# Performance work log

Measured on AMD Instinct MI355X. Metric: run time of the kernel, lower is better.

Reference implementation:

```python
import jax, jax.numpy as jnp
import numpy as np
import math

N, E, H, NB, NL, NG, NELEM = 50000, 800000, 64, 8, 2, 64, 100
CUTOFF = 5.0


def _lin(k, fin, fout):
    kw, kb = jax.random.split(k)
    bound = 1.0 / math.sqrt(fin)
    w = jax.random.uniform(kw, (fin, fout), jnp.float32, -bound, bound)
    b = jax.random.uniform(kb, (fout,), jnp.float32, -bound, bound)
    return w, b


def setup_inputs() -> dict:
    key = jax.random.key(0)
    ks = jax.random.split(key, 12)
    z = jax.random.randint(ks[0], (N,), 0, NELEM)
    pos = jax.random.normal(ks[1], (N, 3), jnp.float32)
    edge_index = jax.random.randint(ks[2], (2, E), 0, N)
    batch = jnp.sort(jax.random.randint(ks[3], (N,), 0, NG))
    embed = jax.random.normal(ks[4], (NELEM, H), jnp.float32)
    # stacked per-interaction MLP params, leading dim = NL
    msg_w1, msg_b1, msg_w2, msg_b2 = [], [], [], []
    upd_w1, upd_b1, upd_w2, upd_b2 = [], [], [], []
    for l in range(NL):
        kl = jax.random.fold_in(ks[5], l)
        k1, k2, k3, k4 = jax.random.split(kl, 4)
        w, b = _lin(k1, 2 * H + NB, H); msg_w1.append(w); msg_b1.append(b)
        w, b = _lin(k2, H, H); msg_w2.append(w); msg_b2.append(b)
        w, b = _lin(k3, 2 * H, H); upd_w1.append(w); upd_b1.append(b)
        w, b = _lin(k4, H, H); upd_w2.append(w); upd_b2.append(b)
    eh_w1, eh_b1 = _lin(ks[6], H, H)
    eh_w2, eh_b2 = _lin(ks[7], H, 1)
    return {
        "z": z, "pos": pos, "edge_index": edge_index, "batch": batch,
        "embed": embed,
        "msg_w1": jnp.stack(msg_w1), "msg_b1": jnp.stack(msg_b1),
        "msg_w2": jnp.stack(msg_w2), "msg_b2": jnp.stack(msg_b2),
        "upd_w1": jnp.stack(upd_w1), "upd_b1": jnp.stack(upd_b1),
        "upd_w2": jnp.stack(upd_w2), "upd_b2": jnp.stack(upd_b2),
        "eh_w1": eh_w1, "eh_b1": eh_b1, "eh_w2": eh_w2, "eh_b2": eh_b2,
    }


def _mace_energy(pos, embed, msg_w1, msg_b1, msg_w2, msg_b2,
                 upd_w1, upd_b1, upd_w2, upd_b2,
                 eh_w1, eh_b1, eh_w2, eh_b2,
                 z, edge_index, batch):
    row, col = edge_index[0], edge_index[1]
    edge_vec = pos[row] - pos[col]                      # (E,3)
    d = jnp.linalg.norm(edge_vec, axis=-1)              # (E,)
    env = jnp.where(d < CUTOFF,
                    jnp.cos(d * (math.pi / (2 * CUTOFF))) ** 2,
                    0.0)
    freqs = jnp.arange(1, NB + 1, dtype=pos.dtype) * (math.pi / CUTOFF)
    d_safe = jnp.where(d > 0, d, 1.0)[:, None]
    edge_attr = jnp.sin(freqs * d[:, None]) / d_safe * env[:, None]  # (E,NB)

    x = embed[z]                                        # (N,H)
    for l in range(NL):
        # PyG source_to_target: x_j = x[row], x_i = x[col], aggregate at col
        msg_in = jnp.concatenate([x[col], x[row], edge_attr], axis=-1)  # (E,2H+NB)
        m = jax.nn.silu(msg_in @ msg_w1[l] + msg_b1[l]) @ msg_w2[l] + msg_b2[l]
        agg = jax.ops.segment_sum(m, col, num_segments=N)               # (N,H)
        u_in = jnp.concatenate([x, agg], axis=-1)
        upd = jax.nn.silu(u_in @ upd_w1[l] + upd_b1[l]) @ upd_w2[l] + upd_b2[l]
        x = x + upd

    atomic_e = jax.nn.silu(x @ eh_w1 + eh_b1) @ eh_w2 + eh_b2           # (N,1)
    energy = jax.ops.segment_sum(atomic_e, batch, num_segments=NG)      # (NG,1)
    return energy.squeeze(-1)


def reference(z, pos, edge_index, batch, embed,
              msg_w1, msg_b1, msg_w2, msg_b2,
              upd_w1, upd_b1, upd_w2, upd_b2,
              eh_w1, eh_b1, eh_w2, eh_b2):
    return _mace_energy(pos, embed, msg_w1, msg_b1, msg_w2, msg_b2,
                        upd_w1, upd_b1, upd_w2, upd_b2,
                        eh_w1, eh_b1, eh_w2, eh_b2,
                        z, edge_index, batch)
```

## Files before the change

kernel.cpp:

```cpp
#include <hip/hip_runtime.h>
#include <math.h>

#define NN 50000
#define EE 800000
#define HH 64
#define NBASIS 8
#define NLAYER 2
#define NGRAPH 64
#define NBLK1 49

using half2_t = decltype(__builtin_amdgcn_cvt_pkrtz(0.0f, 0.0f));
typedef _Float16 f16x8 __attribute__((ext_vector_type(8)));
typedef float f32x4 __attribute__((ext_vector_type(4)));

union U4H8 { uint4 u; f16x8 h; };

__device__ __forceinline__ float silu_f(float v) {
    return v * (1.0f / (1.0f + __expf(-v)));
}

__device__ __forceinline__ unsigned pk2(float a, float b) {
    union { half2_t h; unsigned u; } x;
    x.h = __builtin_amdgcn_cvt_pkrtz(a, b);
    return x.u;
}

__device__ __forceinline__ half2_t u2h(unsigned u) {
    union { unsigned u; half2_t h; } x; x.u = u; return x.h;
}

__global__ __launch_bounds__(256) void prep_k(
    const int* __restrict__ z, const float* __restrict__ embed,
    unsigned* __restrict__ xh,
    const float* __restrict__ msg_w1, const float* __restrict__ msg_w2,
    const float* __restrict__ upd_w1, const float* __restrict__ upd_w2,
    const float* __restrict__ eh_w1,
    unsigned* __restrict__ w1t, unsigned* __restrict__ w2t,
    unsigned* __restrict__ w1tu, unsigned* __restrict__ w2tu,
    unsigned* __restrict__ ehw1t,
    const int* __restrict__ ecol, int* __restrict__ deg,
    float4* __restrict__ agg4)
{
    int b = blockIdx.x;
    if (b < 6250) {
        int idx = b * 256 + threadIdx.x;
        int n = idx >> 5;
        int p = idx & 31;
        const float2* er = (const float2*)(embed + ((size_t)z[n] << 6));
        float2 v = er[p];
        xh[idx] = pk2(v.x, v.y);
    } else if (b < 6362) {
        int idx = (b - 6250) * 256 + threadIdx.x;
        if (idx < 10240) {
            int l = idx / 5120, rem = idx % 5120;
            int f = rem / 80, kp = rem % 80;
            const float* w = msg_w1 + (size_t)l * 136 * 64;
            unsigned v = 0;
            if (kp < 68) v = pk2(w[(2*kp)*64 + f], w[(2*kp+1)*64 + f]);
            w1t[idx] = v;
        } else if (idx < 14336) {
            int j = idx - 10240;
            int l = j / 2048, rem = j % 2048;
            int n = rem / 32, kp = rem % 32;
            const float* w = msg_w2 + (size_t)l * 64 * 64;
            w2t[j] = pk2(w[(2*kp)*64 + n], w[(2*kp+1)*64 + n]);
        } else if (idx < 22528) {
            int j = idx - 14336;
            int l = j / 4096, rem = j % 4096;
            int f = rem >> 6, kp = rem & 63;
            const float* w = upd_w1 + (size_t)l * 128 * 64;
            w1tu[j] = pk2(w[(2*kp)*64 + f], w[(2*kp+1)*64 + f]);
        } else if (idx < 26624) {
            int j = idx - 22528;
            int l = j / 2048, rem = j % 2048;
            int n = rem / 32, kp = rem % 32;
            const float* w = upd_w2 + (size_t)l * 64 * 64;
            w2tu[j] = pk2(w[(2*kp)*64 + n], w[(2*kp+1)*64 + n]);
        } else if (idx < 28672) {
            int j = idx - 26624;
            int f = j / 32, kp = j % 32;
            ehw1t[j] = pk2(eh_w1[(2*kp)*64 + f], eh_w1[(2*kp+1)*64 + f]);
        }
    } else if (b < 9487) {
        int e = (b - 6362) * 256 + threadIdx.x;
        if (e < EE) atomicAdd(&deg[ecol[e]], 1);
    } else {
        int idx = (b - 9487) * 256 + threadIdx.x;
        if (idx < NN * 16) {
            float4 z4; z4.x = z4.y = z4.z = z4.w = 0.0f;
            agg4[idx] = z4;
        }
    }
}

__global__ __launch_bounds__(1024) void scan1_k(
    const int* __restrict__ deg, int* __restrict__ cursor,
    int* __restrict__ bsum)
{
    __shared__ int wsum[16];
    int t = threadIdx.x, lane = t & 63, wave = t >> 6;
    int i = blockIdx.x * 1024 + t;
    int v = (i < NN) ? deg[i] : 0;
    int s = v;
#pragma unroll
    for (int off = 1; off < 64; off <<= 1) {
        int tv = __shfl_up(s, off, 64);
        if (lane >= off) s += tv;
    }
    if (lane == 63) wsum[wave] = s;
    __syncthreads();
    if (wave == 0) {
        int ws = (lane < 16) ? wsum[lane] : 0;
        int ss = ws;
#pragma unroll
        for (int off = 1; off < 16; off <<= 1) {
            int tv = __shfl_up(ss, off, 64);
            if (lane >= off) ss += tv;
        }
        if (lane < 16) wsum[lane] = ss - ws;
    }
    __syncthreads();
    int excl = wsum[wave] + s - v;
    if (i < NN) cursor[i] = excl;
    if (t == 1023) bsum[blockIdx.x] = excl + v;
}

__global__ __launch_bounds__(64) void scan2_k(int* __restrict__ bsum)
{
    int lane = threadIdx.x;
    int v = (lane < NBLK1) ? bsum[lane] : 0;
    int s = v;
#pragma unroll
    for (int off = 1; off < 64; off <<= 1) {
        int tv = __shfl_up(s, off, 64);
        if (lane >= off) s += tv;
    }
    if (lane < NBLK1) bsum[lane] = s - v;
}

__global__ __launch_bounds__(256) void scatter_k(
    const int* __restrict__ erow, const int* __restrict__ ecol,
    const float* __restrict__ pos,
    int* __restrict__ cursor, const int* __restrict__ bsum,
    uint2* __restrict__ edgeS)
{
    int e = blockIdx.x * 256 + threadIdx.x;
    if (e >= EE) return;
    int c = ecol[e], r = erow[e];
    int slot = atomicAdd(&cursor[c], 1) + bsum[c >> 10];
    float dx = pos[3*r]   - pos[3*c];
    float dy = pos[3*r+1] - pos[3*c+1];
    float dz = pos[3*r+2] - pos[3*c+2];
    float d = sqrtf(dx*dx + dy*dy + dz*dz);
    uint2 v;
    v.x = ((unsigned)r << 16) | (unsigned)c;
    v.y = __float_as_uint(d);
    edgeS[slot] = v;
}

__global__ __launch_bounds__(256, 4) void msg_k(
    const uint2* __restrict__ edgeS,
    const unsigned* __restrict__ xh,
    const unsigned* __restrict__ w1t, const float* __restrict__ b1,
    const unsigned* __restrict__ w2t, const float* __restrict__ b2,
    float* __restrict__ agg)
{
    __shared__ unsigned earrT[4][4 * 64];
    __shared__ int ckey_s[4][64];
    __shared__ float Mbuf[4][64 * 34];

    const int wid  = threadIdx.x >> 6;
    const int lane = threadIdx.x & 63;
    const int q = lane >> 4, n15 = lane & 15;
    const size_t base = (size_t)blockIdx.x * 256 + wid * 64;

    uint2 ev = edgeS[base + lane];
    int myrow = (int)(ev.x >> 16);
    int mykey = (int)(ev.x & 0xffffu);
    ckey_s[wid][lane] = mykey;

    int cn[4], rn[4];
#pragma unroll
    for (int nt = 0; nt < 4; ++nt) {
        cn[nt] = __shfl(mykey, nt * 16 + n15, 64);
        rn[nt] = __shfl(myrow, nt * 16 + n15, 64);
    }

    U4H8 bfr[2][4];
#pragma unroll
    for (int nt = 0; nt < 4; ++nt) {
        const uint4* rp = (const uint4*)(xh + ((size_t)rn[nt] << 5));
        bfr[0][nt].u = rp[q];
        bfr[1][nt].u = rp[4 + q];
    }

    {
        float d = __uint_as_float(ev.y);
        float env = 0.0f;
        if (d < 5.0f) {
            float cv = __cosf(d * 0.31415926535897932f);
            env = cv * cv;
        }
        float scale = (d > 0.0f) ? (env / d) : env;
        float ea[NBASIS];
#pragma unroll
        for (int k = 0; k < NBASIS; ++k)
            ea[k] = __sinf((float)(k + 1) * 0.62831853071795865f * d) * scale;
#pragma unroll
        for (int p = 0; p < 4; ++p)
            earrT[wid][p * 64 + lane] = pk2(ea[2*p], ea[2*p+1]);
    }
    int pkk = __shfl_up(mykey, 1, 64);
    unsigned long long bmask = __ballot(lane > 0 && mykey != pkk);
    unsigned m32 = (unsigned)(bmask >> (lane & 32));
    __syncthreads();

    f32x4 acc1[4][4];
#pragma unroll
    for (int mt = 0; mt < 4; ++mt) {
        f32x4 binit = *(const f32x4*)(b1 + mt * 16 + q * 4);
#pragma unroll
        for (int nt = 0; nt < 4; ++nt) acc1[mt][nt] = binit;
    }
#pragma unroll
    for (int ks = 0; ks < 5; ++ks) {
        U4H8 bfk[4];
#pragma unroll
        for (int nt = 0; nt < 4; ++nt) {
            if (ks == 4) {
                int eB = nt * 16 + n15;
                unsigned e0 = earrT[wid][0 * 64 + eB];
                unsigned e1 = earrT[wid][1 * 64 + eB];
                unsigned e2 = earrT[wid][2 * 64 + eB];
                unsigned e3 = earrT[wid][3 * 64 + eB];
                bfk[nt].u.x = (q == 0) ? e0 : 0u;
                bfk[nt].u.y = (q == 0) ? e1 : 0u;
                bfk[nt].u.z = (q == 0) ? e2 : 0u;
                bfk[nt].u.w = (q == 0) ? e3 : 0u;
            } else if (ks < 2) {
                bfk[nt].u = ((const uint4*)(xh + ((size_t)cn[nt] << 5)))[ks * 4 + q];
            } else {
                bfk[nt] = bfr[ks - 2][nt];
            }
        }
#pragma unroll
        for (int mt = 0; mt < 4; ++mt) {
            U4H8 af;
            af.u = *(const uint4*)(w1t + (size_t)(mt * 16 + n15) * 80 + ks * 16 + q * 4);
#pragma unroll
            for (int nt = 0; nt < 4; ++nt)
                acc1[mt][nt] = __builtin_amdgcn_mfma_f32_16x16x32_f16(
                    af.h, bfk[nt].h, acc1[mt][nt], 0, 0, 0);
        }
    }

    unsigned psrc[4][4][2];
#pragma unroll
    for (int mt = 0; mt < 4; ++mt)
#pragma unroll
        for (int nt = 0; nt < 4; ++nt) {
            psrc[mt][nt][0] = pk2(silu_f(acc1[mt][nt][0]), silu_f(acc1[mt][nt][1]));
            psrc[mt][nt][1] = pk2(silu_f(acc1[mt][nt][2]), silu_f(acc1[mt][nt][3]));
        }

    f32x4 acc2[4][4];
#pragma unroll
    for (int nt = 0; nt < 4; ++nt) {
        float b2v = b2[nt * 16 + n15];
        f32x4 binit; binit[0] = b2v; binit[1] = b2v; binit[2] = b2v; binit[3] = b2v;
#pragma unroll
        for (int et = 0; et < 4; ++et) acc2[et][nt] = binit;
    }
#pragma unroll
    for (int ks2 = 0; ks2 < 2; ++ks2) {
        U4H8 wb[4];
#pragma unroll
        for (int nt = 0; nt < 4; ++nt)
            wb[nt].u = *(const uint4*)(w2t + (size_t)(nt * 16 + n15) * 32 + ks2 * 16 + q * 4);
#pragma unroll
        for (int et = 0; et < 4; ++et) {
            unsigned tmp[4];
#pragma unroll
            for (int jr = 0; jr < 4; ++jr) {
                int srcl = (2 * (q & 1) + (jr >> 1)) * 16 + n15;
                unsigned v0 = (unsigned)__shfl((int)psrc[2 * ks2][et][jr & 1], srcl, 64);
                unsigned v1 = (unsigned)__shfl((int)psrc[2 * ks2 + 1][et][jr & 1], srcl, 64);
                tmp[jr] = (q >> 1) ? v1 : v0;
            }
            U4H8 pf;
            pf.u.x = tmp[0]; pf.u.y = tmp[1]; pf.u.z = tmp[2]; pf.u.w = tmp[3];
#pragma unroll
            for (int nt = 0; nt < 4; ++nt)
                acc2[et][nt] = __builtin_amdgcn_mfma_f32_16x16x32_f16(
                    pf.h, wb[nt].h, acc2[et][nt], 0, 0, 0);
        }
    }

#pragma unroll
    for (int hf = 0; hf < 2; ++hf) {
#pragma unroll
        for (int et = 0; et < 4; ++et)
#pragma unroll
            for (int t2 = 0; t2 < 2; ++t2) {
                int nt = 2 * hf + t2;
                int cl = t2 * 16 + n15;
                int eb = et * 16 + q * 4;
#pragma unroll
                for (int r = 0; r < 4; ++r)
                    Mbuf[wid][(eb + r) * 34 + cl] = acc2[et][nt][r];
            }
        __syncthreads();
        {
            int cl = lane & 31, st = lane >> 5;
            int ebase = 32 * st;
            float run = Mbuf[wid][ebase * 34 + cl];
            int runkey = ckey_s[wid][ebase];
            bool atstart = true;
#pragma unroll
            for (int i = 1; i < 32; ++i) {
                float v = Mbuf[wid][(ebase + i) * 34 + cl];
                if ((m32 >> i) & 1u) {
                    float* dst = agg + ((size_t)runkey << 6) + hf * 32 + cl;
                    if (atstart) atomicAdd(dst, run); else *dst = run;
                    runkey = ckey_s[wid][ebase + i]; atstart = false;
                    run = v;
                } else {
                    run += v;
                }
            }
            atomicAdd(agg + ((size_t)runkey << 6) + hf * 32 + cl, run);
        }
        __syncthreads();
    }
}

__global__ __launch_bounds__(256) void upd_k(
    unsigned* __restrict__ xh,
    float* __restrict__ agg,
    const unsigned* __restrict__ w1t, const float* __restrict__ b1,
    const unsigned* __restrict__ w2t, const float* __restrict__ b2,
    const unsigned* __restrict__ ehw1t, const float* __restrict__ ehb1,
    const float* __restrict__ ehw2, const float* __restrict__ ehb2,
    const int* __restrict__ batch, float* __restrict__ energy,
    int do_zero, int do_head)
{
    __shared__ unsigned MU[4][16 * 33];
    __shared__ float esum[NGRAPH];

    const int tid = threadIdx.x;
    const int wid = tid >> 6;
    const int lane = tid & 63;
    const int q = lane >> 4, n15 = lane & 15;
    const int base16 = blockIdx.x * 64 + wid * 16;

    if (do_head) {
        if (tid < NGRAPH) esum[tid] = 0.0f;
        __syncthreads();
    }

    int nodeB = base16 + n15;
    int ncB = (nodeB < NN) ? nodeB : (NN - 1);

    f32x4 acc1[4];
#pragma unroll
    for (int mt = 0; mt < 4; ++mt)
        acc1[mt] = *(const f32x4*)(b1 + mt * 16 + q * 4);
#pragma unroll
    for (int ks = 0; ks < 4; ++ks) {
        U4H8 bfk;
        if (ks < 2) {
            bfk.u = ((const uint4*)(xh + ((size_t)ncB << 5)))[ks * 4 + q];
        } else {
            const float4* ap = (const float4*)(agg + ((size_t)ncB << 6));
            int o = (ks - 2) * 8 + 2 * q;
            float4 a0 = ap[o], a1 = ap[o + 1];
            bfk.u.x = pk2(a0.x, a0.y); bfk.u.y = pk2(a0.z, a0.w);
            bfk.u.z = pk2(a1.x, a1.y); bfk.u.w = pk2(a1.z, a1.w);
        }
#pragma unroll
        for (int mt = 0; mt < 4; ++mt) {
            U4H8 af;
            af.u = *(const uint4*)(w1t + (size_t)(mt * 16 + n15) * 64 + ks * 16 + q * 4);
            acc1[mt] = __builtin_amdgcn_mfma_f32_16x16x32_f16(
                af.h, bfk.h, acc1[mt], 0, 0, 0);
        }
    }

    unsigned psrc[4][2];
#pragma unroll
    for (int mt = 0; mt < 4; ++mt) {
        psrc[mt][0] = pk2(silu_f(acc1[mt][0]), silu_f(acc1[mt][1]));
        psrc[mt][1] = pk2(silu_f(acc1[mt][2]), silu_f(acc1[mt][3]));
    }

    f32x4 acc2[4];
#pragma unroll
    for (int nt = 0; nt < 4; ++nt) {
        float b2v = b2[nt * 16 + n15];
        acc2[nt][0] = b2v; acc2[nt][1] = b2v; acc2[nt][2] = b2v; acc2[nt][3] = b2v;
    }
#pragma unroll
    for (int ks2 = 0; ks2 < 2; ++ks2) {
        unsigned tmp[4];
#pragma unroll
        for (int jr = 0; jr < 4; ++jr) {
            int srcl = (2 * (q & 1) + (jr >> 1)) * 16 + n15;
            unsigned v0 = (unsigned)__shfl((int)psrc[2 * ks2][jr & 1], srcl, 64);
            unsigned v1 = (unsigned)__shfl((int)psrc[2 * ks2 + 1][jr & 1], srcl, 64);
            tmp[jr] = (q >> 1) ? v1 : v0;
        }
        U4H8 pf;
        pf.u.x = tmp[0]; pf.u.y = tmp[1]; pf.u.z = tmp[2]; pf.u.w = tmp[3];
#pragma unroll
        for (int nt = 0; nt < 4; ++nt) {
            U4H8 wb;
            wb.u = *(const uint4*)(w2t + (size_t)(nt * 16 + n15) * 32 + ks2 * 16 + q * 4);
            acc2[nt] = __builtin_amdgcn_mfma_f32_16x16x32_f16(
                pf.h, wb.h, acc2[nt], 0, 0, 0);
        }
    }

#pragma unroll
    for (int nt = 0; nt < 4; ++nt) {
#pragma unroll
        for (int r = 0; r < 4; ++r) {
            int node = base16 + 4 * q + r;
            float vnew = 0.0f;
            if (node < NN) {
                unsigned pu = xh[((size_t)node << 5) + (unsigned)((nt * 16 + n15) >> 1)];
                half2_t hp = u2h(pu);
                float vold = (n15 & 1) ? (float)hp[1] : (float)hp[0];
                vnew = vold + acc2[nt][r];
            }
            float vpart = __shfl_xor(vnew, 1, 64);
            if ((n15 & 1) == 0) {
                unsigned pv = pk2(vnew, vpart);
                int pidx = nt * 8 + (n15 >> 1);
                MU[wid][(4 * q + r) * 33 + pidx] = pv;
                if (node < NN) xh[((size_t)node << 5) + pidx] = pv;
            }
        }
    }

    if (do_zero) {
        if (nodeB < NN) {
            float4 z4; z4.x = z4.y = z4.z = z4.w = 0.0f;
            float4* ap = (float4*)(agg + ((size_t)nodeB << 6));
            ap[2*q] = z4; ap[2*q + 1] = z4;
            ap[8 + 2*q] = z4; ap[8 + 2*q + 1] = z4;
        }
    }

    if (do_head) {
        __syncthreads();
        f32x4 acch[4];
#pragma unroll
        for (int mt = 0; mt < 4; ++mt)
            acch[mt] = *(const f32x4*)(ehb1 + mt * 16 + q * 4);
#pragma unroll
        for (int ks = 0; ks < 2; ++ks) {
            U4H8 bfk;
            bfk.u.x = MU[wid][n15 * 33 + ks * 16 + 4 * q + 0];
            bfk.u.y = MU[wid][n15 * 33 + ks * 16 + 4 * q + 1];
            bfk.u.z = MU[wid][n15 * 33 + ks * 16 + 4 * q + 2];
            bfk.u.w = MU[wid][n15 * 33 + ks * 16 + 4 * q + 3];
#pragma unroll
            for (int mt = 0; mt < 4; ++mt) {
                U4H8 af;
                af.u = *(const uint4*)(ehw1t + (size_t)(mt * 16 + n15) * 32 + ks * 16 + q * 4);
                acch[mt] = __builtin_amdgcn_mfma_f32_16x16x32_f16(
                    af.h, bfk.h, acch[mt], 0, 0, 0);
            }
        }
        f32x4 wv[4];
#pragma unroll
        for (int mt = 0; mt < 4; ++mt)
            wv[mt] = *(const f32x4*)(ehw2 + mt * 16 + q * 4);
        float e = 0.0f;
#pragma unroll
        for (int mt = 0; mt < 4; ++mt)
#pragma unroll
            for (int r = 0; r < 4; ++r)
                e = fmaf(silu_f(acch[mt][r]), wv[mt][r], e);
        e += __shfl_xor(e, 16, 64);
        e += __shfl_xor(e, 32, 64);
        if (q == 0) {
            int node = base16 + n15;
            if (node < NN) atomicAdd(&esum[batch[node]], e + ehb2[0]);
        }
        __syncthreads();
        if (tid < NGRAPH) {
            float v = esum[tid];
            if (v != 0.0f) atomicAdd(energy + tid, v);
        }
    }
}

extern "C" void kernel_launch(void* const* d_in, const int* in_sizes, int n_in,
                              void* d_out, int out_size, void* d_ws, size_t ws_size,
                              hipStream_t stream) {
    const int*   z       = (const int*)  d_in[0];
    const float* pos     = (const float*)d_in[1];
    const int*   eidx    = (const int*)  d_in[2];
    const int*   batch   = (const int*)  d_in[3];
    const float* embed   = (const float*)d_in[4];
    const float* msg_w1  = (const float*)d_in[5];
    const float* msg_b1  = (const float*)d_in[6];
    const float* msg_w2  = (const float*)d_in[7];
    const float* msg_b2  = (const float*)d_in[8];
    const float* upd_w1  = (const float*)d_in[9];
    const float* upd_b1  = (const float*)d_in[10];
    const float* upd_w2  = (const float*)d_in[11];
    const float* upd_b2  = (const float*)d_in[12];
    const float* eh_w1   = (const float*)d_in[13];
    const float* eh_b1   = (const float*)d_in[14];
    const float* eh_w2   = (const float*)d_in[15];
    const float* eh_b2   = (const float*)d_in[16];

    const int* erow = eidx;
    const int* ecol = eidx + EE;

    float*    agg    = (float*)d_ws;
    unsigned* xh     = (unsigned*)(agg + (size_t)NN * HH);
    int*      deg    = (int*)(xh + (size_t)NN * 32);
    int*      cursor = deg + NN;
    int*      bsum   = cursor + NN;
    uint2*    edgeS  = (uint2*)(bsum + 64);
    unsigned* w1t    = (unsigned*)(edgeS + EE);
    unsigned* w2t    = w1t + NLAYER * 64 * 80;
    unsigned* w1tu   = w2t + NLAYER * 64 * 32;
    unsigned* w2tu   = w1tu + NLAYER * 64 * 64;
    unsigned* ehw1t  = w2tu + NLAYER * 64 * 32;
    float*    energy = (float*)d_out;

    (void)hipMemsetAsync(energy, 0, NGRAPH * sizeof(float), stream);
    (void)hipMemsetAsync(deg, 0, NN * sizeof(int), stream);

    prep_k<<<12612, 256, 0, stream>>>(
        z, embed, xh,
        msg_w1, msg_w2, upd_w1, upd_w2, eh_w1,
        w1t, w2t, w1tu, w2tu, ehw1t,
        ecol, deg, (float4*)agg);

    scan1_k<<<NBLK1, 1024, 0, stream>>>(deg, cursor, bsum);
    scan2_k<<<1, 64, 0, stream>>>(bsum);
    scatter_k<<<(EE + 255) / 256, 256, 0, stream>>>(
        erow, ecol, pos, cursor, bsum, edgeS);

    for (int l = 0; l < NLAYER; ++l) {
        msg_k<<<EE / 256, 256, 0, stream>>>(
            edgeS, xh,
            w1t + (size_t)l * 64 * 80,
            msg_b1 + (size_t)l * HH,
            w2t + (size_t)l * 64 * 32,
            msg_b2 + (size_t)l * HH,
            agg);
        upd_k<<<(NN + 63) / 64, 256, 0, stream>>>(
            xh, agg,
            w1tu + (size_t)l * 64 * 64,
            upd_b1 + (size_t)l * HH,
            w2tu + (size_t)l * 64 * 32,
            upd_b2 + (size_t)l * HH,
            ehw1t, eh_b1, eh_w2, eh_b2, batch, energy,
            (l == 0) ? 1 : 0,
            (l == NLAYER - 1) ? 1 : 0);
    }
}
```

Before: 381.0 us.

## Fold message second linear layer into update weights via linearity of aggregation

The message MLP's second linear layer and its bias commute with the segment sum. The per-edge W2 GEMM is therefore removed: msg_k now aggregates silu(hidden) directly, and prep_k precomputes W2·Wu_agg plus the bias term b2·Wu_agg. upd_k adds that bias term scaled by each node's in-degree. This cuts the per-edge MFMA work and shuffles in the dominant message kernel. In exchange, the fused weight is stored in fp16 and the aggregated values change magnitude, which could shift numerical error.

```diff
diff --git a/kernel.cpp b/kernel.cpp
--- a/kernel.cpp
+++ b/kernel.cpp
@@ -33,9 +33,10 @@
     const int* __restrict__ z, const float* __restrict__ embed,
     unsigned* __restrict__ xh,
     const float* __restrict__ msg_w1, const float* __restrict__ msg_w2,
+    const float* __restrict__ msg_b2,
     const float* __restrict__ upd_w1, const float* __restrict__ upd_w2,
     const float* __restrict__ eh_w1,
-    unsigned* __restrict__ w1t, unsigned* __restrict__ w2t,
+    unsigned* __restrict__ w1t, float* __restrict__ vbuf,
     unsigned* __restrict__ w1tu, unsigned* __restrict__ w2tu,
     unsigned* __restrict__ ehw1t,
     const int* __restrict__ ecol, int* __restrict__ deg,
@@ -59,17 +60,33 @@
             if (kp < 68) v = pk2(w[(2*kp)*64 + f], w[(2*kp+1)*64 + f]);
             w1t[idx] = v;
         } else if (idx < 14336) {
-            int j = idx - 10240;
-            int l = j / 2048, rem = j % 2048;
-            int n = rem / 32, kp = rem % 32;
-            const float* w = msg_w2 + (size_t)l * 64 * 64;
-            w2t[j] = pk2(w[(2*kp)*64 + n], w[(2*kp+1)*64 + n]);
         } else if (idx < 22528) {
             int j = idx - 14336;
             int l = j / 4096, rem = j % 4096;
             int f = rem >> 6, kp = rem & 63;
             const float* w = upd_w1 + (size_t)l * 128 * 64;
-            w1tu[j] = pk2(w[(2*kp)*64 + f], w[(2*kp+1)*64 + f]);
+            unsigned outv;
+            if (kp < 32) {
+                outv = pk2(w[(2*kp)*64 + f], w[(2*kp+1)*64 + f]);
+            } else {
+                const float* w2m = msg_w2 + (size_t)l * 64 * 64;
+                int j0 = 2 * kp - 64;
+                float v0 = 0.0f, v1 = 0.0f;
+                for (int k = 0; k < 64; ++k) {
+                    float wa = w[(64 + k) * 64 + f];
+                    v0 += w2m[j0 * 64 + k]       * wa;
+                    v1 += w2m[(j0 + 1) * 64 + k] * wa;
+                }
+                outv = pk2(v0, v1);
+                if (kp == 63) {
+                    const float* b2m = msg_b2 + (size_t)l * 64;
+                    float s = 0.0f;
+                    for (int k = 0; k < 64; ++k)
+                        s += b2m[k] * w[(64 + k) * 64 + f];
+                    vbuf[l * 64 + f] = s;
+                }
+            }
+            w1tu[j] = outv;
         } else if (idx < 26624) {
             int j = idx - 22528;
             int l = j / 2048, rem = j % 2048;
@@ -162,7 +179,6 @@
     const uint2* __restrict__ edgeS,
     const unsigned* __restrict__ xh,
     const unsigned* __restrict__ w1t, const float* __restrict__ b1,
-    const unsigned* __restrict__ w2t, const float* __restrict__ b2,
     float* __restrict__ agg)
 {
     __shared__ unsigned earrT[4][4 * 64];
@@ -254,61 +270,20 @@
         }
     }
 
-    unsigned psrc[4][4][2];
-#pragma unroll
-    for (int mt = 0; mt < 4; ++mt)
-#pragma unroll
-        for (int nt = 0; nt < 4; ++nt) {
-            psrc[mt][nt][0] = pk2(silu_f(acc1[mt][nt][0]), silu_f(acc1[mt][nt][1]));
-            psrc[mt][nt][1] = pk2(silu_f(acc1[mt][nt][2]), silu_f(acc1[mt][nt][3]));
-        }
-
-    f32x4 acc2[4][4];
-#pragma unroll
-    for (int nt = 0; nt < 4; ++nt) {
-        float b2v = b2[nt * 16 + n15];
-        f32x4 binit; binit[0] = b2v; binit[1] = b2v; binit[2] = b2v; binit[3] = b2v;
-#pragma unroll
-        for (int et = 0; et < 4; ++et) acc2[et][nt] = binit;
-    }
-#pragma unroll
-    for (int ks2 = 0; ks2 < 2; ++ks2) {
-        U4H8 wb[4];
-#pragma unroll
-        for (int nt = 0; nt < 4; ++nt)
-            wb[nt].u = *(const uint4*)(w2t + (size_t)(nt * 16 + n15) * 32 + ks2 * 16 + q * 4);
-#pragma unroll
-        for (int et = 0; et < 4; ++et) {
-            unsigned tmp[4];
-#pragma unroll
-            for (int jr = 0; jr < 4; ++jr) {
-                int srcl = (2 * (q & 1) + (jr >> 1)) * 16 + n15;
-                unsigned v0 = (unsigned)__shfl((int)psrc[2 * ks2][et][jr & 1], srcl, 64);
-                unsigned v1 = (unsigned)__shfl((int)psrc[2 * ks2 + 1][et][jr & 1], srcl, 64);
-                tmp[jr] = (q >> 1) ? v1 : v0;
-            }
-            U4H8 pf;
-            pf.u.x = tmp[0]; pf.u.y = tmp[1]; pf.u.z = tmp[2]; pf.u.w = tmp[3];
-#pragma unroll
-            for (int nt = 0; nt < 4; ++nt)
-                acc2[et][nt] = __builtin_amdgcn_mfma_f32_16x16x32_f16(
-                    pf.h, wb[nt].h, acc2[et][nt], 0, 0, 0);
-        }
-    }
-
 #pragma unroll
     for (int hf = 0; hf < 2; ++hf) {
 #pragma unroll
-        for (int et = 0; et < 4; ++et)
-#pragma unroll
-            for (int t2 = 0; t2 < 2; ++t2) {
-                int nt = 2 * hf + t2;
-                int cl = t2 * 16 + n15;
-                int eb = et * 16 + q * 4;
+        for (int mh = 0; mh < 2; ++mh) {
+            int mt = 2 * hf + mh;
+#pragma unroll
+            for (int nt = 0; nt < 4; ++nt) {
+                int eb = nt * 16 + n15;
 #pragma unroll
                 for (int r = 0; r < 4; ++r)
-                    Mbuf[wid][(eb + r) * 34 + cl] = acc2[et][nt][r];
-            }
+                    Mbuf[wid][eb * 34 + mh * 16 + q * 4 + r] =
+                        silu_f(acc1[mt][nt][r]);
+            }
+        }
         __syncthreads();
         {
             int cl = lane & 31, st = lane >> 5;
@@ -338,6 +313,7 @@
     unsigned* __restrict__ xh,
     float* __restrict__ agg,
     const unsigned* __restrict__ w1t, const float* __restrict__ b1,
+    const float* __restrict__ vb, const int* __restrict__ deg,
     const unsigned* __restrict__ w2t, const float* __restrict__ b2,
     const unsigned* __restrict__ ehw1t, const float* __restrict__ ehb1,
     const float* __restrict__ ehw2, const float* __restrict__ ehb2,
@@ -361,10 +337,16 @@
     int nodeB = base16 + n15;
     int ncB = (nodeB < NN) ? nodeB : (NN - 1);
 
+    float degf = (float)deg[ncB];
     f32x4 acc1[4];
 #pragma unroll
-    for (int mt = 0; mt < 4; ++mt)
-        acc1[mt] = *(const f32x4*)(b1 + mt * 16 + q * 4);
+    for (int mt = 0; mt < 4; ++mt) {
+        f32x4 bi = *(const f32x4*)(b1 + mt * 16 + q * 4);
+        f32x4 vv = *(const f32x4*)(vb + mt * 16 + q * 4);
+#pragma unroll
+        for (int r = 0; r < 4; ++r) bi[r] = fmaf(degf, vv[r], bi[r]);
+        acc1[mt] = bi;
+    }
 #pragma unroll
     for (int ks = 0; ks < 4; ++ks) {
         U4H8 bfk;
@@ -531,6 +513,7 @@
     unsigned* w1tu   = w2t + NLAYER * 64 * 32;
     unsigned* w2tu   = w1tu + NLAYER * 64 * 64;
     unsigned* ehw1t  = w2tu + NLAYER * 64 * 32;
+    float*    vbuf   = (float*)w2t;
     float*    energy = (float*)d_out;
 
     (void)hipMemsetAsync(energy, 0, NGRAPH * sizeof(float), stream);
@@ -538,8 +521,8 @@
 
     prep_k<<<12612, 256, 0, stream>>>(
         z, embed, xh,
-        msg_w1, msg_w2, upd_w1, upd_w2, eh_w1,
-        w1t, w2t, w1tu, w2tu, ehw1t,
+        msg_w1, msg_w2, msg_b2, upd_w1, upd_w2, eh_w1,
+        w1t, vbuf, w1tu, w2tu, ehw1t,
         ecol, deg, (float4*)agg);
 
     scan1_k<<<NBLK1, 1024, 0, stream>>>(deg, cursor, bsum);
@@ -552,13 +535,13 @@
             edgeS, xh,
             w1t + (size_t)l * 64 * 80,
             msg_b1 + (size_t)l * HH,
-            w2t + (size_t)l * 64 * 32,
-            msg_b2 + (size_t)l * HH,
             agg);
         upd_k<<<(NN + 63) / 64, 256, 0, stream>>>(
             xh, agg,
             w1tu + (size_t)l * 64 * 64,
             upd_b1 + (size_t)l * HH,
+            vbuf + (size_t)l * 64,
+            deg,
             w2tu + (size_t)l * 64 * 32,
             upd_b2 + (size_t)l * HH,
             ehw1t, eh_b1, eh_w2, eh_b2, batch, energy,
```

Result: faster. 357.9 us (-6.1%).
